# Kernel tuning notes

Hardware: AMD Instinct MI355X
Metric: run time of the kernel (lower is better)

## Reference

```python
import jax, jax.numpy as jnp
import numpy as np
import math

B, S, D, H, L, FF, T = 2, 1024, 1024, 16, 8, 4096, 512
HD = D // H
EPS = 1e-5


def _ln(x, g, b):
    m = jnp.mean(x, axis=-1, keepdims=True)
    v = jnp.var(x, axis=-1, keepdims=True)
    return (x - m) * jax.lax.rsqrt(v + EPS) * g + b


def _rope(x, cos, sin):
    # x: [B,S,H,HD]; interleaved even/odd rotary as in _apply_rotary_emb_sincos
    xe, xo = x[..., 0::2], x[..., 1::2]
    c = cos[None, :, None, :]
    s = sin[None, :, None, :]
    return jnp.stack([xe * c - xo * s, xe * s + xo * c], axis=-1).reshape(x.shape)


def setup_inputs():
    key = jax.random.key(0)
    ks = iter(jax.random.split(key, 40))
    n = lambda shape, sc=0.02: jax.random.normal(next(ks), shape, jnp.float32) * sc
    return {
        "inputs_embeds": jax.random.normal(next(ks), (B, S, D), jnp.float32),
        "attention_mask": jnp.ones((B, 1, 1, S), jnp.float32),
        "time_step": jax.random.uniform(next(ks), (B,), jnp.float32),
        "wpe": n((S, D)),
        "ln1_g": jnp.ones((L, D)), "ln1_b": jnp.zeros((L, D)),
        "attn_w": n((L, D, 3 * D)), "attn_b": jnp.zeros((L, 3 * D)),
        "projw": n((L, D, D)), "projb": jnp.zeros((L, D)),
        "ln2_g": jnp.ones((L, D)), "ln2_b": jnp.zeros((L, D)),
        "fcw": n((L, D, FF)), "fcb": jnp.zeros((L, FF)),
        "pw2": n((L, FF, D)), "pb2": jnp.zeros((L, D)),
        "sst": n((L, 6, D), 1.0 / D ** 0.5),
        "te_w1": n((T, D)), "te_b1": jnp.zeros((D,)),
        "te_w2": n((D, D)), "te_b2": jnp.zeros((D,)),
        "ada_w": n((D, 6 * D)), "ada_b": jnp.zeros((6 * D,)),
        "lnf_g": jnp.ones((D,)), "lnf_b": jnp.zeros((D,)),
        "fsst": n((2, D), 1.0 / D ** 0.5),
        "out_w": n((D, D)), "out_b": jnp.zeros((D,)),
    }


def reference(inputs_embeds, attention_mask, time_step, wpe, ln1_g, ln1_b,
              attn_w, attn_b, projw, projb, ln2_g, ln2_b, fcw, fcb, pw2, pb2,
              sst, te_w1, te_b1, te_w2, te_b2, ada_w, ada_b, lnf_g, lnf_b,
              fsst, out_w, out_b):
    hs = inputs_embeds + wpe[:S][None]  # position embedding
    # rotary tables: [S, HD//2]
    half = HD // 2
    freqs = 1.0 / (10000.0 ** (jnp.arange(half, dtype=jnp.float32) * 2.0 / HD))
    ang = jnp.arange(S, dtype=jnp.float32)[:, None] * freqs[None]
    cos, sin = jnp.cos(ang), jnp.sin(ang)
    mask = (1.0 - attention_mask) * jnp.finfo(jnp.float32).min  # [B,1,1,S]
    # timestep embedding (flow_t_size=T, scale=1000, max_period=10000)
    halfT = T // 2
    tf = jnp.exp(-math.log(10000.0) * jnp.arange(halfT, dtype=jnp.float32) / halfT)
    targs = time_step[:, None] * tf[None] * 1000.0
    tproj = jnp.concatenate([jnp.cos(targs), jnp.sin(targs)], axis=-1)  # [B,T]
    emb = jax.nn.silu(tproj @ te_w1 + te_b1) @ te_w2 + te_b2  # [B,D]
    adaln = (jax.nn.silu(emb) @ ada_w + ada_b).reshape(B, 6, D)

    layer_params = dict(ln1_g=ln1_g, ln1_b=ln1_b, aw=attn_w, ab=attn_b,
                        pw=projw, pb=projb, ln2_g=ln2_g, ln2_b=ln2_b,
                        fw=fcw, fb=fcb, qw=pw2, qb=pb2, sst=sst)

    def block(h, p):
        mod = p["sst"][None] + adaln  # [B,6,D]
        sh1, sc1, g1, sh2, sc2, g2 = [mod[:, i:i + 1] for i in range(6)]
        res = h
        x = _ln(h, p["ln1_g"], p["ln1_b"]) * (1.0 + sc1) + sh1
        qkv = x @ p["aw"] + p["ab"]
        q, k, v = [t.reshape(B, S, H, HD) for t in jnp.split(qkv, 3, axis=-1)]
        q, k = _rope(q, cos, sin), _rope(k, cos, sin)
        scores = jnp.einsum("bqhd,bkhd->bhqk", q, k) / math.sqrt(HD) + mask
        attn = jax.nn.softmax(scores, axis=-1)
        o = jnp.einsum("bhqk,bkhd->bqhd", attn, v).reshape(B, S, D)
        o = o @ p["pw"] + p["pb"]
        h = o * g1 + res
        res = h
        x = _ln(h, p["ln2_g"], p["ln2_b"]) * (1.0 + sc2) + sh2
        x = jax.nn.gelu(x @ p["fw"] + p["fb"], approximate=True) @ p["qw"] + p["qb"]
        return x * g2 + res, None

    hs, _ = jax.lax.scan(block, hs, layer_params)
    fmod = fsst[None] + emb[:, None]  # [B,2,D]
    shift, scale = fmod[:, 0:1], fmod[:, 1:2]
    hs = _ln(hs, lnf_g, lnf_b) * (1.0 + scale) + shift
    return hs @ out_w + out_b
```

## Files before the change

### kernel.cpp

```cpp
#include <hip/hip_runtime.h>
#include <stdint.h>

typedef unsigned short u16;
typedef __attribute__((ext_vector_type(8))) short bf8_t;
typedef __attribute__((ext_vector_type(4))) float f4_t;

#define DEV static __device__ __forceinline__
#define MFMA16(a, b, c) __builtin_amdgcn_mfma_f32_16x16x32_bf16((a), (b), (c), 0, 0, 0)
#define GLDS(gp, lp) __builtin_amdgcn_global_load_lds((const __attribute__((address_space(1))) void*)(gp), \
                                                      (__attribute__((address_space(3))) void*)(lp), 16, 0, 0)

DEV u16 f2bf(float f) {
  union { float f; uint32_t u; } x; x.f = f;
  uint32_t r = x.u + 0x7FFFu + ((x.u >> 16) & 1u);
  return (u16)(r >> 16);
}

DEV void transpose_body(const float* __restrict__ W, u16* __restrict__ WT, int K, int N,
                        int n0, int k0, u16 (*tl)[66]) {
  const int t = threadIdx.x;
  const int tx = t & 15, ty = t >> 4;
  #pragma unroll
  for (int i = 0; i < 64; i += 16) {
    const float4 v = *(const float4*)&W[(long)(k0 + ty + i) * N + n0 + tx * 4];
    tl[tx * 4 + 0][ty + i] = f2bf(v.x);
    tl[tx * 4 + 1][ty + i] = f2bf(v.y);
    tl[tx * 4 + 2][ty + i] = f2bf(v.z);
    tl[tx * 4 + 3][ty + i] = f2bf(v.w);
  }
  __syncthreads();
  const int c = t & 15, r = t >> 4;
  #pragma unroll
  for (int i = 0; i < 64; i += 16) {
    const u16* p = &tl[r + i][c * 4];
    uint2 w;
    w.x = (uint32_t)p[0] | ((uint32_t)p[1] << 16);
    w.y = (uint32_t)p[2] | ((uint32_t)p[3] << 16);
    *(uint2*)&WT[(long)(n0 + r + i) * K + k0 + c * 4] = w;
  }
}

__global__ __launch_bounds__(256) void transpose_k(const float* __restrict__ W, u16* __restrict__ WT,
                                                   int K, int N) {
  __shared__ u16 tl[64][66];
  transpose_body(W, WT, K, N, blockIdx.x * 64, blockIdx.y * 64, tl);
}

__global__ __launch_bounds__(256)
void transpose4_k(const float* __restrict__ w0, u16* __restrict__ o0,
                  const float* __restrict__ w1, u16* __restrict__ o1,
                  const float* __restrict__ w2, u16* __restrict__ o2,
                  const float* __restrict__ w3, u16* __restrict__ o3) {
  __shared__ u16 tl[64][66];
  int bid = blockIdx.x;
  const float* W; u16* O; int K, N, nbx;
  if (bid < 768)        {             W = w0; O = o0; K = 1024; N = 3072; nbx = 48; }
  else if (bid < 1024)  { bid -= 768; W = w1; O = o1; K = 1024; N = 1024; nbx = 16; }
  else if (bid < 2048)  { bid -= 1024; W = w2; O = o2; K = 1024; N = 4096; nbx = 64; }
  else                  { bid -= 2048; W = w3; O = o3; K = 4096; N = 1024; nbx = 16; }
  transpose_body(W, O, K, N, (bid % nbx) * 64, (bid / nbx) * 64, tl);
}

enum { EPI_F32 = 0, EPI_GATE = 1, EPI_GELU = 2, EPI_RAW = 3 };

template <int BM, int EPI, int KS>
__global__ __launch_bounds__(256)
void gemm_bt(const u16* __restrict__ A, const u16* __restrict__ BT, const float* __restrict__ bias,
             float* outF, u16* outB, const float* gate, const float* res, int M, int N, int K) {
  constexpr int MI = BM / 32;
  __shared__ u16 sA[BM * 32];
  __shared__ u16 sB[128 * 32];
  const int tid = threadIdx.x, lane = tid & 63, wid = tid >> 6;
  const long rowBase = (long)blockIdx.x * BM;
  const long colBase = (long)blockIdx.y * 128;
  const int kz = (KS > 1) ? blockIdx.z : 0;
  const int kbeg = kz * (K / KS), kend = kbeg + K / KS;
  const int wr = (wid >> 1) * (BM / 2), wc = (wid & 1) * 64;
  const int fr = lane & 15, kg = (lane >> 4) * 8;

  const f4_t zero = {0.0f, 0.0f, 0.0f, 0.0f};
  f4_t acc[MI][4];
  #pragma unroll
  for (int i = 0; i < MI; ++i)
    #pragma unroll
    for (int j = 0; j < 4; ++j) acc[i][j] = zero;

  const int sr = lane >> 2, scol = (lane & 3) * 8;
  const int c0 = wid * 2;
  const u16 *Ag0, *Ag1 = nullptr, *Bg0, *Bg1;
  u16 *lA0, *lA1 = nullptr, *lB0, *lB1;
  if constexpr (BM == 128) {
    Ag0 = A + (rowBase + c0 * 16 + sr) * (long)K + scol;
    Ag1 = A + (rowBase + c0 * 16 + 16 + sr) * (long)K + scol;
    lA0 = &sA[(c0 * 16) * 32];
    lA1 = &sA[(c0 * 16 + 16) * 32];
  } else {
    Ag0 = A + (rowBase + wid * 16 + sr) * (long)K + scol;
    lA0 = &sA[(wid * 16) * 32];
  }
  Bg0 = BT + (colBase + c0 * 16 + sr) * (long)K + scol;
  Bg1 = BT + (colBase + c0 * 16 + 16 + sr) * (long)K + scol;
  lB0 = &sB[(c0 * 16) * 32];
  lB1 = &sB[(c0 * 16 + 16) * 32];

  for (int k0 = kbeg; k0 < kend; k0 += 32) {
    GLDS(Ag0 + k0, lA0);
    if constexpr (BM == 128) GLDS(Ag1 + k0, lA1);
    GLDS(Bg0 + k0, lB0);
    GLDS(Bg1 + k0, lB1);
    __syncthreads();
    bf8_t af[MI], bfv[4];
    #pragma unroll
    for (int m = 0; m < MI; ++m) af[m] = *(const bf8_t*)&sA[(wr + m * 16 + fr) * 32 + kg];
    #pragma unroll
    for (int n = 0; n < 4; ++n) bfv[n] = *(const bf8_t*)&sB[(wc + n * 16 + fr) * 32 + kg];
    #pragma unroll
    for (int m = 0; m < MI; ++m)
      #pragma unroll
      for (int n = 0; n < 4; ++n) acc[m][n] = MFMA16(af[m], bfv[n], acc[m][n]);
    __syncthreads();
  }

  const int r0 = (lane >> 4) * 4;
  #pragma unroll
  for (int m = 0; m < MI; ++m) {
    #pragma unroll
    for (int n = 0; n < 4; ++n) {
      const long col = colBase + wc + n * 16 + fr;
      const float bv = (EPI == EPI_RAW) ? 0.0f : bias[col];
      #pragma unroll
      for (int j = 0; j < 4; ++j) {
        const long row = rowBase + wr + m * 16 + r0 + j;
        float v = acc[m][n][j] + bv;
        if (EPI == EPI_F32) {
          outF[row * N + col] = v;
        } else if (EPI == EPI_RAW) {
          outF[((long)kz * M + row) * N + col] = v;
        } else if (EPI == EPI_GATE) {
          const int b = (int)(row >> 10);
          const float g = gate[(long)b * 6144 + col];
          outF[row * N + col] = v * g + res[row * N + col];
        } else {
          const float t = 0.7978845608028654f * (v + 0.044715f * v * v * v);
          const float e = __expf(2.0f * t);
          const float th = 1.0f - 2.0f / (e + 1.0f);
          outB[row * N + col] = f2bf(0.5f * v * (1.0f + th));
        }
      }
    }
  }
}

__global__ __launch_bounds__(256)
void reduce_gate(const float* __restrict__ part, const float* __restrict__ bias,
                 const float* __restrict__ gate, float* __restrict__ hs) {
  const long i = (long)blockIdx.x * 256 + threadIdx.x;
  const long e0 = i * 4;
  const int col = (int)(e0 & 1023);
  const int row = (int)(e0 >> 10);
  const int b = row >> 10;
  const f4_t p = *(const f4_t*)&part[e0];
  const f4_t q = *(const f4_t*)&part[e0 + 2048ll * 1024];
  const f4_t bv = *(const f4_t*)&bias[col];
  const f4_t gv = *(const f4_t*)&gate[(long)b * 6144 + col];
  const f4_t r = *(const f4_t*)&hs[e0];
  f4_t o;
  #pragma unroll
  for (int j = 0; j < 4; ++j) o[j] = (p[j] + q[j] + bv[j]) * gv[j] + r[j];
  *(f4_t*)&hs[e0] = o;
}

__global__ __launch_bounds__(256)
void ln_mod(const float* __restrict__ h, const float* __restrict__ gamma, const float* __restrict__ beta,
            const float* shp, const float* scp, int bstride, u16* __restrict__ xb) {
  __shared__ float red[8];
  const int row = blockIdx.x;
  const int b = row >> 10;
  const int t = threadIdx.x;
  const float* hp = h + (long)row * 1024;
  float4 x = *(const float4*)&hp[t * 4];
  float s = x.x + x.y + x.z + x.w;
  #pragma unroll
  for (int o = 32; o > 0; o >>= 1) s += __shfl_down(s, o);
  const int lane = t & 63, wid = t >> 6;
  if (lane == 0) red[wid] = s;
  __syncthreads();
  const float mean = (red[0] + red[1] + red[2] + red[3]) * 0.0009765625f;
  const float d0 = x.x - mean, d1 = x.y - mean, d2 = x.z - mean, d3 = x.w - mean;
  float vs = d0 * d0 + d1 * d1 + d2 * d2 + d3 * d3;
  #pragma unroll
  for (int o = 32; o > 0; o >>= 1) vs += __shfl_down(vs, o);
  if (lane == 0) red[4 + wid] = vs;
  __syncthreads();
  const float var = (red[4] + red[5] + red[6] + red[7]) * 0.0009765625f;
  const float inv = rsqrtf(var + 1e-5f);
  const int d = t * 4;
  const float4 gg = *(const float4*)&gamma[d];
  const float4 bb = *(const float4*)&beta[d];
  const float4 sh = *(const float4*)&shp[(long)b * bstride + d];
  const float4 sc = *(const float4*)&scp[(long)b * bstride + d];
  union { u16 u[4]; uint2 v; } pk;
  pk.u[0] = f2bf((d0 * inv * gg.x + bb.x) * (1.0f + sc.x) + sh.x);
  pk.u[1] = f2bf((d1 * inv * gg.y + bb.y) * (1.0f + sc.y) + sh.y);
  pk.u[2] = f2bf((d2 * inv * gg.z + bb.z) * (1.0f + sc.z) + sh.z);
  pk.u[3] = f2bf((d3 * inv * gg.w + bb.w) * (1.0f + sc.w) + sh.w);
  *(uint2*)&xb[(long)row * 1024 + d] = pk.v;
}

__global__ __launch_bounds__(256)
void rope_split(const float* __restrict__ qkv, const float* __restrict__ ct, const float* __restrict__ st,
                u16* __restrict__ qb, u16* __restrict__ kb) {
  const int row = blockIdx.x;
  const int b = row >> 10, s = row & 1023;
  const float* rp = qkv + (long)row * 3072;
  const int t = threadIdx.x;
  #pragma unroll
  for (int which = 0; which < 2; ++which) {
    const float* xp = rp + which * 1024;
    u16* op = which ? kb : qb;
    #pragma unroll
    for (int j = 0; j < 2; ++j) {
      const int p = t + j * 256;
      const int h = p >> 5, i = p & 31;
      const float xe = xp[h * 64 + 2 * i], xo = xp[h * 64 + 2 * i + 1];
      const float c = ct[s * 32 + i], sn = st[s * 32 + i];
      const long base = (((long)(b * 16 + h)) * 1024 + s) * 64 + 2 * i;
      op[base] = f2bf(xe * c - xo * sn);
      op[base + 1] = f2bf(xe * sn + xo * c);
    }
  }
}

__global__ __launch_bounds__(256)
void v_transpose(const float* __restrict__ qkv, u16* __restrict__ vt) {
  __shared__ u16 tl[64][66];
  const int s0 = blockIdx.x * 64;
  const int h = blockIdx.y, b = blockIdx.z;
  const int t = threadIdx.x;
  const int tx = t & 15, ty = t >> 4;
  #pragma unroll
  for (int i = 0; i < 64; i += 16) {
    const float4 v = *(const float4*)&qkv[(long)(b * 1024 + s0 + ty + i) * 3072 + 2048 + h * 64 + tx * 4];
    tl[tx * 4 + 0][ty + i] = f2bf(v.x);
    tl[tx * 4 + 1][ty + i] = f2bf(v.y);
    tl[tx * 4 + 2][ty + i] = f2bf(v.z);
    tl[tx * 4 + 3][ty + i] = f2bf(v.w);
  }
  __syncthreads();
  const int c = t & 15, r = t >> 4;
  #pragma unroll
  for (int i = 0; i < 64; i += 16) {
    const u16* p = &tl[r + i][c * 4];
    uint2 w;
    w.x = (uint32_t)p[0] | ((uint32_t)p[1] << 16);
    w.y = (uint32_t)p[2] | ((uint32_t)p[3] << 16);
    *(uint2*)&vt[((long)(b * 16 + h) * 64 + r + i) * 1024 + s0 + c * 4] = w;
  }
}

DEV void attn_body(bf8_t (&kcur)[4][2], bf8_t (&knxt)[4][2], const bf8_t (&qf)[2],
                   f4_t (&oacc)[4], float& m, float& psum, int kc,
                   const u16* __restrict__ Kp, const u16* __restrict__ Vt,
                   const float* smadd, u16* myP, int fr, int g) {
  const f4_t zero = {0.0f, 0.0f, 0.0f, 0.0f};
  bf8_t vf[4][2];
  #pragma unroll
  for (int dt = 0; dt < 4; ++dt)
    #pragma unroll
    for (int ks = 0; ks < 2; ++ks)
      vf[dt][ks] = *(const bf8_t*)&Vt[(long)(dt * 16 + fr) * 1024 + kc + ks * 32 + g * 8];
  f4_t st[4];
  #pragma unroll
  for (int kt = 0; kt < 4; ++kt) {
    st[kt] = MFMA16(kcur[kt][0], qf[0], zero);
    st[kt] = MFMA16(kcur[kt][1], qf[1], st[kt]);
  }
  {
    const int kn = (kc + 64) & 1023;
    #pragma unroll
    for (int kt = 0; kt < 4; ++kt)
      #pragma unroll
      for (int dh = 0; dh < 2; ++dh)
        knxt[kt][dh] = *(const bf8_t*)&Kp[(long)(kn + kt * 16 + fr) * 64 + dh * 32 + g * 8];
  }
  float p[4][4];
  float cm = -3.402823466e38f;
  #pragma unroll
  for (int kt = 0; kt < 4; ++kt)
    #pragma unroll
    for (int j = 0; j < 4; ++j) {
      p[kt][j] = st[kt][j] * 0.125f + smadd[kc + kt * 16 + g * 4 + j];
      cm = fmaxf(cm, p[kt][j]);
    }
  cm = fmaxf(cm, __shfl_xor(cm, 16));
  cm = fmaxf(cm, __shfl_xor(cm, 32));
  const float nm = fmaxf(m, cm);
  const float sc = __expf(m - nm);
  m = nm;
  float ls = 0.0f;
  #pragma unroll
  for (int kt = 0; kt < 4; ++kt)
    #pragma unroll
    for (int j = 0; j < 4; ++j) {
      p[kt][j] = __expf(p[kt][j] - nm);
      ls += p[kt][j];
    }
  psum = psum * sc + ls;
  #pragma unroll
  for (int dt = 0; dt < 4; ++dt)
    #pragma unroll
    for (int j = 0; j < 4; ++j) oacc[dt][j] *= sc;
  #pragma unroll
  for (int kt = 0; kt < 4; ++kt) {
    const int kb = kt * 2 + (g >> 1);
    uint2 w;
    w.x = (uint32_t)f2bf(p[kt][0]) | ((uint32_t)f2bf(p[kt][1]) << 16);
    w.y = (uint32_t)f2bf(p[kt][2]) | ((uint32_t)f2bf(p[kt][3]) << 16);
    *(uint2*)&myP[(kb * 16 + fr) * 8 + (g & 1) * 4] = w;
  }
  bf8_t pa0 = *(const bf8_t*)&myP[(g * 16 + fr) * 8];
  bf8_t pa1 = *(const bf8_t*)&myP[((4 + g) * 16 + fr) * 8];
  #pragma unroll
  for (int dt = 0; dt < 4; ++dt) {
    oacc[dt] = MFMA16(vf[dt][0], pa0, oacc[dt]);
    oacc[dt] = MFMA16(vf[dt][1], pa1, oacc[dt]);
  }
}

__global__ __launch_bounds__(256)
void attn_k(const u16* __restrict__ qb, const u16* __restrict__ kb, const u16* __restrict__ vt,
            const float* __restrict__ amask, u16* __restrict__ ob) {
  __shared__ float smadd[1024];
  __shared__ u16 pl[4][1024];
  const int q0 = blockIdx.x * 64;
  const int h = blockIdx.y, b = blockIdx.z;
  const long bh = b * 16 + h;
  const int tid = threadIdx.x, lane = tid & 63, wid = tid >> 6;
  const int fr = lane & 15, g = lane >> 4;

  for (int i = tid; i < 1024; i += 256)
    smadd[i] = (1.0f - amask[b * 1024 + i]) * -3.402823466e38f;
  __syncthreads();

  const u16* Q = qb + (bh * 1024 + q0 + wid * 16) * 64;
  const u16* Kp = kb + bh * 1024 * 64;
  const u16* Vt = vt + bh * 64 * 1024;
  u16* myP = &pl[wid][0];

  bf8_t qf[2];
  qf[0] = *(const bf8_t*)&Q[fr * 64 + g * 8];
  qf[1] = *(const bf8_t*)&Q[fr * 64 + 32 + g * 8];

  const f4_t zero = {0.0f, 0.0f, 0.0f, 0.0f};
  f4_t oacc[4];
  #pragma unroll
  for (int dt = 0; dt < 4; ++dt) oacc[dt] = zero;
  float m = -1e30f, psum = 0.0f;

  bf8_t kfA[4][2], kfB[4][2];
  #pragma unroll
  for (int kt = 0; kt < 4; ++kt)
    #pragma unroll
    for (int dh = 0; dh < 2; ++dh)
      kfA[kt][dh] = *(const bf8_t*)&Kp[(long)(kt * 16 + fr) * 64 + dh * 32 + g * 8];

  for (int kc = 0; kc < 1024; kc += 128) {
    attn_body(kfA, kfB, qf, oacc, m, psum, kc, Kp, Vt, smadd, myP, fr, g);
    attn_body(kfB, kfA, qf, oacc, m, psum, kc + 64, Kp, Vt, smadd, myP, fr, g);
  }

  float ts = psum + __shfl_xor(psum, 16);
  ts += __shfl_xor(ts, 32);
  const float inv = 1.0f / ts;
  const long qrow = (long)b * 1024 + q0 + wid * 16 + fr;
  #pragma unroll
  for (int dt = 0; dt < 4; ++dt) {
    union { u16 u[4]; uint2 v; } pk;
    #pragma unroll
    for (int j = 0; j < 4; ++j) pk.u[j] = f2bf(oacc[dt][j] * inv);
    *(uint2*)&ob[qrow * 1024 + h * 64 + dt * 16 + g * 4] = pk.v;
  }
}

__global__ void rope_tables(float* ct, float* st) {
  const int i = blockIdx.x * 256 + threadIdx.x;
  const int s = i >> 5, k = i & 31;
  const float freq = __expf(-9.210340371976184f * (float)(2 * k) / 64.0f);
  const float a = (float)s * freq;
  ct[i] = cosf(a);
  st[i] = sinf(a);
}

__global__ void init_hs(const float* __restrict__ e, const float* __restrict__ wpe, float* __restrict__ hs) {
  const long i = (long)blockIdx.x * 256 + threadIdx.x;
  float4 a = ((const float4*)e)[i];
  const float4 w = ((const float4*)wpe)[i & 262143];
  a.x += w.x; a.y += w.y; a.z += w.z; a.w += w.w;
  ((float4*)hs)[i] = a;
}

__global__ void time_proj_k(const float* __restrict__ ts, float* __restrict__ tproj) {
  const int j = blockIdx.x * 256 + threadIdx.x;
  const int b = blockIdx.y;
  const float tf = __expf(-9.210340371976184f * (float)(j & 255) / 256.0f);
  const float a = ts[b] * tf * 1000.0f;
  tproj[b * 512 + j] = (j < 256) ? cosf(a) : sinf(a);
}

__global__ __launch_bounds__(256)
void time_mlp1(const float* __restrict__ tproj, const float* __restrict__ w1,
               const float* __restrict__ b1, float* __restrict__ h1) {
  __shared__ float red[8][32];
  const int dl = threadIdx.x & 31, sl = threadIdx.x >> 5;
  const int d = blockIdx.x * 32 + dl, b = blockIdx.y;
  float acc = 0.0f;
  for (int j = sl * 64; j < sl * 64 + 64; ++j) acc += tproj[b * 512 + j] * w1[(long)j * 1024 + d];
  red[sl][dl] = acc;
  __syncthreads();
  if (threadIdx.x < 32) {
    const int dd = blockIdx.x * 32 + threadIdx.x;
    float a = b1[dd];
    #pragma unroll
    for (int s = 0; s < 8; ++s) a += red[s][threadIdx.x];
    h1[b * 1024 + dd] = a / (1.0f + __expf(-a));
  }
}

__global__ __launch_bounds__(256)
void time_mlp2(const float* __restrict__ h1, const float* __restrict__ w2,
               const float* __restrict__ b2, float* __restrict__ emb) {
  __shared__ float red[8][32];
  const int dl = threadIdx.x & 31, sl = threadIdx.x >> 5;
  const int d = blockIdx.x * 32 + dl, b = blockIdx.y;
  float acc = 0.0f;
  for (int j = sl * 128; j < sl * 128 + 128; ++j) acc += h1[b * 1024 + j] * w2[(long)j * 1024 + d];
  red[sl][dl] = acc;
  __syncthreads();
  if (threadIdx.x < 32) {
    const int dd = blockIdx.x * 32 + threadIdx.x;
    float a = b2[dd];
    #pragma unroll
    for (int s = 0; s < 8; ++s) a += red[s][threadIdx.x];
    emb[b * 1024 + dd] = a;
  }
}

__global__ void silu_k(const float* __restrict__ in, float* __restrict__ out, int n) {
  const int i = blockIdx.x * 256 + threadIdx.x;
  if (i < n) { const float v = in[i]; out[i] = v / (1.0f + __expf(-v)); }
}

__global__ void adaln_part(const float* __restrict__ se, const float* __restrict__ aw,
                           float* __restrict__ part) {
  const int j = blockIdx.x * 256 + threadIdx.x;
  const int b = blockIdx.y, kz = blockIdx.z;
  float acc = 0.0f;
  for (int k = kz * 128; k < kz * 128 + 128; ++k) acc += se[b * 1024 + k] * aw[(long)k * 6144 + j];
  part[((long)kz * 2 + b) * 6144 + j] = acc;
}

__global__ void adaln_reduce(const float* __restrict__ part, const float* __restrict__ ab,
                             float* __restrict__ adaln) {
  const int j = blockIdx.x * 256 + threadIdx.x;
  const int b = blockIdx.y;
  float acc = ab[j];
  #pragma unroll
  for (int kz = 0; kz < 8; ++kz) acc += part[((long)kz * 2 + b) * 6144 + j];
  adaln[b * 6144 + j] = acc;
}

__global__ void build_mods(const float* __restrict__ sst, const float* __restrict__ adaln,
                           const float* __restrict__ fsst, const float* __restrict__ emb,
                           float* __restrict__ modAll, float* __restrict__ fmod) {
  const int i = blockIdx.x * 256 + threadIdx.x;
  if (i < 98304) {
    const int d = i & 1023;
    const int rest = i >> 10;
    const int slot = rest % 6;
    const int t2 = rest / 6;
    const int bb = t2 & 1, l = t2 >> 1;
    modAll[i] = sst[(long)(l * 6 + slot) * 1024 + d] + adaln[bb * 6144 + slot * 1024 + d];
  } else if (i < 98304 + 4096) {
    const int j = i - 98304;
    const int d = j & 1023;
    const int slot = (j >> 10) & 1;
    const int bb = j >> 11;
    fmod[j] = fsst[slot * 1024 + d] + emb[bb * 1024 + d];
  }
}

extern "C" void kernel_launch(void* const* d_in, const int* in_sizes, int n_in,
                              void* d_out, int out_size, void* d_ws, size_t ws_size,
                              hipStream_t stream) {
  const float* inp_emb = (const float*)d_in[0];
  const float* amask  = (const float*)d_in[1];
  const float* tstep  = (const float*)d_in[2];
  const float* wpe    = (const float*)d_in[3];
  const float* ln1_g  = (const float*)d_in[4];
  const float* ln1_b  = (const float*)d_in[5];
  const float* attn_w = (const float*)d_in[6];
  const float* attn_b = (const float*)d_in[7];
  const float* projw  = (const float*)d_in[8];
  const float* projb  = (const float*)d_in[9];
  const float* ln2_g  = (const float*)d_in[10];
  const float* ln2_b  = (const float*)d_in[11];
  const float* fcw    = (const float*)d_in[12];
  const float* fcb    = (const float*)d_in[13];
  const float* pw2    = (const float*)d_in[14];
  const float* pb2    = (const float*)d_in[15];
  const float* sst    = (const float*)d_in[16];
  const float* te_w1  = (const float*)d_in[17];
  const float* te_b1  = (const float*)d_in[18];
  const float* te_w2  = (const float*)d_in[19];
  const float* te_b2  = (const float*)d_in[20];
  const float* ada_w  = (const float*)d_in[21];
  const float* ada_b  = (const float*)d_in[22];
  const float* lnf_g  = (const float*)d_in[23];
  const float* lnf_b  = (const float*)d_in[24];
  const float* fsst   = (const float*)d_in[25];
  const float* out_w  = (const float*)d_in[26];
  const float* out_b  = (const float*)d_in[27];
  float* out = (float*)d_out;
  (void)in_sizes; (void)n_in; (void)out_size; (void)ws_size;

  char* wsb = (char*)d_ws;
  size_t off = 0;
  auto alloc = [&](size_t bytes) -> void* {
    void* p = wsb + off;
    off += (bytes + 255) & ~(size_t)255;
    return p;
  };
  u16* wtA = (u16*)alloc(3072ll * 1024 * 2);
  u16* wtP = (u16*)alloc(1024ll * 1024 * 2);
  u16* wtF = (u16*)alloc(4096ll * 1024 * 2);
  u16* wtQ = (u16*)alloc(1024ll * 4096 * 2);
  u16* wtO = (u16*)alloc(1024ll * 1024 * 2);
  float* hs   = (float*)alloc(2048ll * 1024 * 4);
  float* qkv  = (float*)alloc(2048ll * 3072 * 4);
  u16*   ffb  = (u16*)qkv;
  float* part = (float*)alloc(2ll * 2048 * 1024 * 4);
  u16* xb = (u16*)alloc(2048ll * 1024 * 2);
  u16* qb = (u16*)alloc(2048ll * 1024 * 2);
  u16* kb = (u16*)alloc(2048ll * 1024 * 2);
  u16* vt = (u16*)alloc(2048ll * 1024 * 2);
  u16* ob = (u16*)alloc(2048ll * 1024 * 2);
  float* ct    = (float*)alloc(32768 * 4);
  float* st    = (float*)alloc(32768 * 4);
  float* tproj = (float*)alloc(2 * 512 * 4);
  float* h1    = (float*)alloc(2 * 1024 * 4);
  float* emb   = (float*)alloc(2 * 1024 * 4);
  float* se    = (float*)alloc(2 * 1024 * 4);
  float* adaln = (float*)alloc(2 * 6144 * 4);
  float* modAll = (float*)alloc(8ll * 2 * 6 * 1024 * 4);
  float* fmod   = (float*)alloc(2 * 2 * 1024 * 4);

  rope_tables<<<128, 256, 0, stream>>>(ct, st);
  init_hs<<<2048, 256, 0, stream>>>(inp_emb, wpe, hs);
  time_proj_k<<<dim3(2, 2), 256, 0, stream>>>(tstep, tproj);
  time_mlp1<<<dim3(32, 2), 256, 0, stream>>>(tproj, te_w1, te_b1, h1);
  time_mlp2<<<dim3(32, 2), 256, 0, stream>>>(h1, te_w2, te_b2, emb);
  silu_k<<<8, 256, 0, stream>>>(emb, se, 2048);
  adaln_part<<<dim3(24, 2, 8), 256, 0, stream>>>(se, ada_w, part);
  adaln_reduce<<<dim3(24, 2), 256, 0, stream>>>(part, ada_b, adaln);
  build_mods<<<400, 256, 0, stream>>>(sst, adaln, fsst, emb, modAll, fmod);
  transpose_k<<<dim3(16, 16), 256, 0, stream>>>(out_w, wtO, 1024, 1024);

  for (int l = 0; l < 8; ++l) {
    const float* ml = modAll + (long)l * 12288;
    transpose4_k<<<3072, 256, 0, stream>>>(attn_w + (long)l * 1024 * 3072, wtA,
                                           projw + (long)l * 1024 * 1024, wtP,
                                           fcw + (long)l * 1024 * 4096, wtF,
                                           pw2 + (long)l * 4096 * 1024, wtQ);

    ln_mod<<<2048, 256, 0, stream>>>(hs, ln1_g + l * 1024, ln1_b + l * 1024,
                                     ml + 0 * 1024, ml + 1 * 1024, 6144, xb);
    gemm_bt<128, EPI_F32, 1><<<dim3(16, 24), 256, 0, stream>>>(xb, wtA, attn_b + l * 3072,
                                                               qkv, nullptr, nullptr, nullptr, 2048, 3072, 1024);
    rope_split<<<2048, 256, 0, stream>>>(qkv, ct, st, qb, kb);
    v_transpose<<<dim3(16, 16, 2), 256, 0, stream>>>(qkv, vt);
    attn_k<<<dim3(16, 16, 2), 256, 0, stream>>>(qb, kb, vt, amask, ob);
    gemm_bt<64, EPI_GATE, 1><<<dim3(32, 8), 256, 0, stream>>>(ob, wtP, projb + l * 1024,
                                                              hs, nullptr, ml + 2 * 1024, hs, 2048, 1024, 1024);
    ln_mod<<<2048, 256, 0, stream>>>(hs, ln2_g + l * 1024, ln2_b + l * 1024,
                                     ml + 3 * 1024, ml + 4 * 1024, 6144, xb);
    gemm_bt<128, EPI_GELU, 1><<<dim3(16, 32), 256, 0, stream>>>(xb, wtF, fcb + l * 4096,
                                                                nullptr, ffb, nullptr, nullptr, 2048, 4096, 1024);
    gemm_bt<128, EPI_RAW, 2><<<dim3(16, 8, 2), 256, 0, stream>>>(ffb, wtQ, nullptr,
                                                                 part, nullptr, nullptr, nullptr, 2048, 1024, 4096);
    reduce_gate<<<2048, 256, 0, stream>>>(part, pb2 + l * 1024, ml + 5 * 1024, hs);
  }

  ln_mod<<<2048, 256, 0, stream>>>(hs, lnf_g, lnf_b, fmod + 0, fmod + 1024, 2048, xb);
  gemm_bt<64, EPI_F32, 1><<<dim3(32, 8), 256, 0, stream>>>(xb, wtO, out_b,
                                                           out, nullptr, nullptr, nullptr, 2048, 1024, 1024);
}
```

Baseline: 1.951 ms.

## Double-buffer GEMM LDS, fuse reduce-gate with next LayerNorm, shrink attention blocks

Adds a two-buffer LDS pipeline to the bf16 GEMM so the next K-tile's global-to-LDS load is issued before the current tile's MFMAs. The FF2 split-K reduction is fused with the following LayerNorm (the next layer's ln1 or the final LN), which removes one read and write pass over the hidden state per layer. LayerNorm now runs one wave per row with xor-shuffle reductions instead of a block-wide reduction through shared memory. Attention switches to one-wave blocks of 16 query rows with vectorized mask loads, and the rope writes are packed into 32-bit stores. The GEMM loop keeps a single barrier per iteration, and since global_load_lds is asynchronous, whether the prefetch is properly waited on before it is read is a correctness risk.

After: 1.826 ms. 1.07x faster.

```diff
diff --git a/kernel.cpp b/kernel.cpp
--- a/kernel.cpp
+++ b/kernel.cpp
@@ -68,13 +68,13 @@
 void gemm_bt(const u16* __restrict__ A, const u16* __restrict__ BT, const float* __restrict__ bias,
              float* outF, u16* outB, const float* gate, const float* res, int M, int N, int K) {
   constexpr int MI = BM / 32;
-  __shared__ u16 sA[BM * 32];
-  __shared__ u16 sB[128 * 32];
+  __shared__ u16 sA[2][BM * 32];
+  __shared__ u16 sB[2][128 * 32];
   const int tid = threadIdx.x, lane = tid & 63, wid = tid >> 6;
   const long rowBase = (long)blockIdx.x * BM;
   const long colBase = (long)blockIdx.y * 128;
   const int kz = (KS > 1) ? blockIdx.z : 0;
-  const int kbeg = kz * (K / KS), kend = kbeg + K / KS;
+  const int kbeg = kz * (K / KS);
   const int wr = (wid >> 1) * (BM / 2), wc = (wid & 1) * 64;
   const int fr = lane & 15, kg = (lane >> 4) * 8;
 
@@ -88,37 +88,45 @@
   const int sr = lane >> 2, scol = (lane & 3) * 8;
   const int c0 = wid * 2;
   const u16 *Ag0, *Ag1 = nullptr, *Bg0, *Bg1;
-  u16 *lA0, *lA1 = nullptr, *lB0, *lB1;
+  int aoff0, aoff1 = 0, boff0, boff1;
   if constexpr (BM == 128) {
     Ag0 = A + (rowBase + c0 * 16 + sr) * (long)K + scol;
     Ag1 = A + (rowBase + c0 * 16 + 16 + sr) * (long)K + scol;
-    lA0 = &sA[(c0 * 16) * 32];
-    lA1 = &sA[(c0 * 16 + 16) * 32];
+    aoff0 = (c0 * 16) * 32;
+    aoff1 = (c0 * 16 + 16) * 32;
   } else {
     Ag0 = A + (rowBase + wid * 16 + sr) * (long)K + scol;
-    lA0 = &sA[(wid * 16) * 32];
+    aoff0 = (wid * 16) * 32;
   }
   Bg0 = BT + (colBase + c0 * 16 + sr) * (long)K + scol;
   Bg1 = BT + (colBase + c0 * 16 + 16 + sr) * (long)K + scol;
-  lB0 = &sB[(c0 * 16) * 32];
-  lB1 = &sB[(c0 * 16 + 16) * 32];
-
-  for (int k0 = kbeg; k0 < kend; k0 += 32) {
-    GLDS(Ag0 + k0, lA0);
-    if constexpr (BM == 128) GLDS(Ag1 + k0, lA1);
-    GLDS(Bg0 + k0, lB0);
-    GLDS(Bg1 + k0, lB1);
-    __syncthreads();
+  boff0 = (c0 * 16) * 32;
+  boff1 = (c0 * 16 + 16) * 32;
+
+  auto stage = [&](int buf, int k0) {
+    GLDS(Ag0 + k0, &sA[buf][aoff0]);
+    if constexpr (BM == 128) GLDS(Ag1 + k0, &sA[buf][aoff1]);
+    GLDS(Bg0 + k0, &sB[buf][boff0]);
+    GLDS(Bg1 + k0, &sB[buf][boff1]);
+  };
+
+  const int nk = (K / KS) / 32;
+  stage(0, kbeg);
+  __syncthreads();
+  int cur = 0;
+  for (int t = 0; t < nk; ++t) {
+    if (t + 1 < nk) stage(cur ^ 1, kbeg + (t + 1) * 32);
     bf8_t af[MI], bfv[4];
     #pragma unroll
-    for (int m = 0; m < MI; ++m) af[m] = *(const bf8_t*)&sA[(wr + m * 16 + fr) * 32 + kg];
-    #pragma unroll
-    for (int n = 0; n < 4; ++n) bfv[n] = *(const bf8_t*)&sB[(wc + n * 16 + fr) * 32 + kg];
+    for (int m = 0; m < MI; ++m) af[m] = *(const bf8_t*)&sA[cur][(wr + m * 16 + fr) * 32 + kg];
+    #pragma unroll
+    for (int n = 0; n < 4; ++n) bfv[n] = *(const bf8_t*)&sB[cur][(wc + n * 16 + fr) * 32 + kg];
     #pragma unroll
     for (int m = 0; m < MI; ++m)
       #pragma unroll
       for (int n = 0; n < 4; ++n) acc[m][n] = MFMA16(af[m], bfv[n], acc[m][n]);
     __syncthreads();
+    cur ^= 1;
   }
 
   const int r0 = (lane >> 4) * 4;
@@ -152,59 +160,95 @@
 }
 
 __global__ __launch_bounds__(256)
-void reduce_gate(const float* __restrict__ part, const float* __restrict__ bias,
-                 const float* __restrict__ gate, float* __restrict__ hs) {
-  const long i = (long)blockIdx.x * 256 + threadIdx.x;
-  const long e0 = i * 4;
-  const int col = (int)(e0 & 1023);
-  const int row = (int)(e0 >> 10);
-  const int b = row >> 10;
-  const f4_t p = *(const f4_t*)&part[e0];
-  const f4_t q = *(const f4_t*)&part[e0 + 2048ll * 1024];
-  const f4_t bv = *(const f4_t*)&bias[col];
-  const f4_t gv = *(const f4_t*)&gate[(long)b * 6144 + col];
-  const f4_t r = *(const f4_t*)&hs[e0];
-  f4_t o;
-  #pragma unroll
-  for (int j = 0; j < 4; ++j) o[j] = (p[j] + q[j] + bv[j]) * gv[j] + r[j];
-  *(f4_t*)&hs[e0] = o;
-}
-
-__global__ __launch_bounds__(256)
 void ln_mod(const float* __restrict__ h, const float* __restrict__ gamma, const float* __restrict__ beta,
             const float* shp, const float* scp, int bstride, u16* __restrict__ xb) {
-  __shared__ float red[8];
-  const int row = blockIdx.x;
+  const int row = blockIdx.x * 4 + (threadIdx.x >> 6);
+  const int lane = threadIdx.x & 63;
   const int b = row >> 10;
-  const int t = threadIdx.x;
-  const float* hp = h + (long)row * 1024;
-  float4 x = *(const float4*)&hp[t * 4];
-  float s = x.x + x.y + x.z + x.w;
-  #pragma unroll
-  for (int o = 32; o > 0; o >>= 1) s += __shfl_down(s, o);
-  const int lane = t & 63, wid = t >> 6;
-  if (lane == 0) red[wid] = s;
-  __syncthreads();
-  const float mean = (red[0] + red[1] + red[2] + red[3]) * 0.0009765625f;
-  const float d0 = x.x - mean, d1 = x.y - mean, d2 = x.z - mean, d3 = x.w - mean;
-  float vs = d0 * d0 + d1 * d1 + d2 * d2 + d3 * d3;
-  #pragma unroll
-  for (int o = 32; o > 0; o >>= 1) vs += __shfl_down(vs, o);
-  if (lane == 0) red[4 + wid] = vs;
-  __syncthreads();
-  const float var = (red[4] + red[5] + red[6] + red[7]) * 0.0009765625f;
-  const float inv = rsqrtf(var + 1e-5f);
-  const int d = t * 4;
-  const float4 gg = *(const float4*)&gamma[d];
-  const float4 bb = *(const float4*)&beta[d];
-  const float4 sh = *(const float4*)&shp[(long)b * bstride + d];
-  const float4 sc = *(const float4*)&scp[(long)b * bstride + d];
-  union { u16 u[4]; uint2 v; } pk;
-  pk.u[0] = f2bf((d0 * inv * gg.x + bb.x) * (1.0f + sc.x) + sh.x);
-  pk.u[1] = f2bf((d1 * inv * gg.y + bb.y) * (1.0f + sc.y) + sh.y);
-  pk.u[2] = f2bf((d2 * inv * gg.z + bb.z) * (1.0f + sc.z) + sh.z);
-  pk.u[3] = f2bf((d3 * inv * gg.w + bb.w) * (1.0f + sc.w) + sh.w);
-  *(uint2*)&xb[(long)row * 1024 + d] = pk.v;
+  const long base = (long)row * 1024;
+  f4_t x[4];
+  float s = 0.0f;
+  #pragma unroll
+  for (int j = 0; j < 4; ++j) {
+    x[j] = *(const f4_t*)&h[base + j * 256 + lane * 4];
+    s += x[j][0] + x[j][1] + x[j][2] + x[j][3];
+  }
+  #pragma unroll
+  for (int o = 32; o > 0; o >>= 1) s += __shfl_xor(s, o);
+  const float mean = s * 0.0009765625f;
+  float vs = 0.0f;
+  #pragma unroll
+  for (int j = 0; j < 4; ++j)
+    #pragma unroll
+    for (int e = 0; e < 4; ++e) { const float d = x[j][e] - mean; vs += d * d; }
+  #pragma unroll
+  for (int o = 32; o > 0; o >>= 1) vs += __shfl_xor(vs, o);
+  const float inv = rsqrtf(vs * 0.0009765625f + 1e-5f);
+  #pragma unroll
+  for (int j = 0; j < 4; ++j) {
+    const int col = j * 256 + lane * 4;
+    const f4_t gg = *(const f4_t*)&gamma[col];
+    const f4_t bb = *(const f4_t*)&beta[col];
+    const f4_t sh = *(const f4_t*)&shp[(long)b * bstride + col];
+    const f4_t sc = *(const f4_t*)&scp[(long)b * bstride + col];
+    union { u16 u[4]; uint2 v; } pk;
+    #pragma unroll
+    for (int e = 0; e < 4; ++e)
+      pk.u[e] = f2bf(((x[j][e] - mean) * inv * gg[e] + bb[e]) * (1.0f + sc[e]) + sh[e]);
+    *(uint2*)&xb[base + col] = pk.v;
+  }
+}
+
+__global__ __launch_bounds__(256)
+void reduce_gate_ln(const float* __restrict__ part, const float* __restrict__ bias,
+                    const float* __restrict__ gate, float* __restrict__ hs,
+                    const float* __restrict__ gamma, const float* __restrict__ beta,
+                    const float* shp, const float* scp, int bstride, u16* __restrict__ xb) {
+  const int row = blockIdx.x * 4 + (threadIdx.x >> 6);
+  const int lane = threadIdx.x & 63;
+  const int b = row >> 10;
+  const long base = (long)row * 1024;
+  f4_t v[4];
+  float s = 0.0f;
+  #pragma unroll
+  for (int j = 0; j < 4; ++j) {
+    const int col = j * 256 + lane * 4;
+    const f4_t p = *(const f4_t*)&part[base + col];
+    const f4_t q = *(const f4_t*)&part[2048ll * 1024 + base + col];
+    const f4_t bv = *(const f4_t*)&bias[col];
+    const f4_t gv = *(const f4_t*)&gate[(long)b * 6144 + col];
+    const f4_t r = *(const f4_t*)&hs[base + col];
+    f4_t o;
+    #pragma unroll
+    for (int e = 0; e < 4; ++e) o[e] = (p[e] + q[e] + bv[e]) * gv[e] + r[e];
+    *(f4_t*)&hs[base + col] = o;
+    v[j] = o;
+    s += o[0] + o[1] + o[2] + o[3];
+  }
+  #pragma unroll
+  for (int o = 32; o > 0; o >>= 1) s += __shfl_xor(s, o);
+  const float mean = s * 0.0009765625f;
+  float vs = 0.0f;
+  #pragma unroll
+  for (int j = 0; j < 4; ++j)
+    #pragma unroll
+    for (int e = 0; e < 4; ++e) { const float d = v[j][e] - mean; vs += d * d; }
+  #pragma unroll
+  for (int o = 32; o > 0; o >>= 1) vs += __shfl_xor(vs, o);
+  const float inv = rsqrtf(vs * 0.0009765625f + 1e-5f);
+  #pragma unroll
+  for (int j = 0; j < 4; ++j) {
+    const int col = j * 256 + lane * 4;
+    const f4_t gg = *(const f4_t*)&gamma[col];
+    const f4_t bb = *(const f4_t*)&beta[col];
+    const f4_t sh = *(const f4_t*)&shp[(long)b * bstride + col];
+    const f4_t sc = *(const f4_t*)&scp[(long)b * bstride + col];
+    union { u16 u[4]; uint2 v; } pk;
+    #pragma unroll
+    for (int e = 0; e < 4; ++e)
+      pk.u[e] = f2bf(((v[j][e] - mean) * inv * gg[e] + bb[e]) * (1.0f + sc[e]) + sh[e]);
+    *(uint2*)&xb[base + col] = pk.v;
+  }
 }
 
 __global__ __launch_bounds__(256)
@@ -222,11 +266,12 @@
     for (int j = 0; j < 2; ++j) {
       const int p = t + j * 256;
       const int h = p >> 5, i = p & 31;
-      const float xe = xp[h * 64 + 2 * i], xo = xp[h * 64 + 2 * i + 1];
+      const float2 xx = *(const float2*)&xp[h * 64 + 2 * i];
       const float c = ct[s * 32 + i], sn = st[s * 32 + i];
       const long base = (((long)(b * 16 + h)) * 1024 + s) * 64 + 2 * i;
-      op[base] = f2bf(xe * c - xo * sn);
-      op[base + 1] = f2bf(xe * sn + xo * c);
+      const uint32_t w = (uint32_t)f2bf(xx.x * c - xx.y * sn) |
+                         ((uint32_t)f2bf(xx.x * sn + xx.y * c) << 16);
+      *(uint32_t*)&op[base] = w;
     }
   }
 }
@@ -286,12 +331,14 @@
   float p[4][4];
   float cm = -3.402823466e38f;
   #pragma unroll
-  for (int kt = 0; kt < 4; ++kt)
+  for (int kt = 0; kt < 4; ++kt) {
+    const f4_t ma = *(const f4_t*)&smadd[kc + kt * 16 + g * 4];
     #pragma unroll
     for (int j = 0; j < 4; ++j) {
-      p[kt][j] = st[kt][j] * 0.125f + smadd[kc + kt * 16 + g * 4 + j];
+      p[kt][j] = st[kt][j] * 0.125f + ma[j];
       cm = fmaxf(cm, p[kt][j]);
     }
+  }
   cm = fmaxf(cm, __shfl_xor(cm, 16));
   cm = fmaxf(cm, __shfl_xor(cm, 32));
   const float nm = fmaxf(m, cm);
@@ -327,25 +374,30 @@
   }
 }
 
-__global__ __launch_bounds__(256)
+__global__ __launch_bounds__(64)
 void attn_k(const u16* __restrict__ qb, const u16* __restrict__ kb, const u16* __restrict__ vt,
             const float* __restrict__ amask, u16* __restrict__ ob) {
   __shared__ float smadd[1024];
-  __shared__ u16 pl[4][1024];
-  const int q0 = blockIdx.x * 64;
+  __shared__ u16 pl[1024];
+  const int q0 = blockIdx.x * 16;
   const int h = blockIdx.y, b = blockIdx.z;
   const long bh = b * 16 + h;
-  const int tid = threadIdx.x, lane = tid & 63, wid = tid >> 6;
+  const int lane = threadIdx.x;
   const int fr = lane & 15, g = lane >> 4;
 
-  for (int i = tid; i < 1024; i += 256)
-    smadd[i] = (1.0f - amask[b * 1024 + i]) * -3.402823466e38f;
-  __syncthreads();
-
-  const u16* Q = qb + (bh * 1024 + q0 + wid * 16) * 64;
+  #pragma unroll
+  for (int i = 0; i < 4; ++i) {
+    const int e = (lane + i * 64) * 4;
+    const f4_t am = *(const f4_t*)&amask[b * 1024 + e];
+    f4_t md;
+    #pragma unroll
+    for (int j = 0; j < 4; ++j) md[j] = (1.0f - am[j]) * -3.402823466e38f;
+    *(f4_t*)&smadd[e] = md;
+  }
+
+  const u16* Q = qb + (bh * 1024 + q0) * 64;
   const u16* Kp = kb + bh * 1024 * 64;
   const u16* Vt = vt + bh * 64 * 1024;
-  u16* myP = &pl[wid][0];
 
   bf8_t qf[2];
   qf[0] = *(const bf8_t*)&Q[fr * 64 + g * 8];
@@ -365,14 +417,14 @@
       kfA[kt][dh] = *(const bf8_t*)&Kp[(long)(kt * 16 + fr) * 64 + dh * 32 + g * 8];
 
   for (int kc = 0; kc < 1024; kc += 128) {
-    attn_body(kfA, kfB, qf, oacc, m, psum, kc, Kp, Vt, smadd, myP, fr, g);
-    attn_body(kfB, kfA, qf, oacc, m, psum, kc + 64, Kp, Vt, smadd, myP, fr, g);
+    attn_body(kfA, kfB, qf, oacc, m, psum, kc, Kp, Vt, smadd, pl, fr, g);
+    attn_body(kfB, kfA, qf, oacc, m, psum, kc + 64, Kp, Vt, smadd, pl, fr, g);
   }
 
   float ts = psum + __shfl_xor(psum, 16);
   ts += __shfl_xor(ts, 32);
   const float inv = 1.0f / ts;
-  const long qrow = (long)b * 1024 + q0 + wid * 16 + fr;
+  const long qrow = (long)b * 1024 + q0 + fr;
   #pragma unroll
   for (int dt = 0; dt < 4; ++dt) {
     union { u16 u[4]; uint2 v; } pk;
@@ -565,6 +617,8 @@
   build_mods<<<400, 256, 0, stream>>>(sst, adaln, fsst, emb, modAll, fmod);
   transpose_k<<<dim3(16, 16), 256, 0, stream>>>(out_w, wtO, 1024, 1024);
 
+  ln_mod<<<512, 256, 0, stream>>>(hs, ln1_g, ln1_b, modAll + 0 * 1024, modAll + 1 * 1024, 6144, xb);
+
   for (int l = 0; l < 8; ++l) {
     const float* ml = modAll + (long)l * 12288;
     transpose4_k<<<3072, 256, 0, stream>>>(attn_w + (long)l * 1024 * 3072, wtA,
@@ -572,25 +626,30 @@
                                            fcw + (long)l * 1024 * 4096, wtF,
                                            pw2 + (long)l * 4096 * 1024, wtQ);
 
-    ln_mod<<<2048, 256, 0, stream>>>(hs, ln1_g + l * 1024, ln1_b + l * 1024,
-                                     ml + 0 * 1024, ml + 1 * 1024, 6144, xb);
     gemm_bt<128, EPI_F32, 1><<<dim3(16, 24), 256, 0, stream>>>(xb, wtA, attn_b + l * 3072,
                                                                qkv, nullptr, nullptr, nullptr, 2048, 3072, 1024);
     rope_split<<<2048, 256, 0, stream>>>(qkv, ct, st, qb, kb);
     v_transpose<<<dim3(16, 16, 2), 256, 0, stream>>>(qkv, vt);
-    attn_k<<<dim3(16, 16, 2), 256, 0, stream>>>(qb, kb, vt, amask, ob);
+    attn_k<<<dim3(64, 16, 2), 64, 0, stream>>>(qb, kb, vt, amask, ob);
     gemm_bt<64, EPI_GATE, 1><<<dim3(32, 8), 256, 0, stream>>>(ob, wtP, projb + l * 1024,
                                                               hs, nullptr, ml + 2 * 1024, hs, 2048, 1024, 1024);
-    ln_mod<<<2048, 256, 0, stream>>>(hs, ln2_g + l * 1024, ln2_b + l * 1024,
-                                     ml + 3 * 1024, ml + 4 * 1024, 6144, xb);
+    ln_mod<<<512, 256, 0, stream>>>(hs, ln2_g + l * 1024, ln2_b + l * 1024,
+                                    ml + 3 * 1024, ml + 4 * 1024, 6144, xb);
     gemm_bt<128, EPI_GELU, 1><<<dim3(16, 32), 256, 0, stream>>>(xb, wtF, fcb + l * 4096,
                                                                 nullptr, ffb, nullptr, nullptr, 2048, 4096, 1024);
     gemm_bt<128, EPI_RAW, 2><<<dim3(16, 8, 2), 256, 0, stream>>>(ffb, wtQ, nullptr,
                                                                  part, nullptr, nullptr, nullptr, 2048, 1024, 4096);
-    reduce_gate<<<2048, 256, 0, stream>>>(part, pb2 + l * 1024, ml + 5 * 1024, hs);
-  }
-
-  ln_mod<<<2048, 256, 0, stream>>>(hs, lnf_g, lnf_b, fmod + 0, fmod + 1024, 2048, xb);
+    if (l < 7) {
+      const float* mln = modAll + (long)(l + 1) * 12288;
+      reduce_gate_ln<<<512, 256, 0, stream>>>(part, pb2 + l * 1024, ml + 5 * 1024, hs,
+                                              ln1_g + (l + 1) * 1024, ln1_b + (l + 1) * 1024,
+                                              mln + 0 * 1024, mln + 1 * 1024, 6144, xb);
+    } else {
+      reduce_gate_ln<<<512, 256, 0, stream>>>(part, pb2 + l * 1024, ml + 5 * 1024, hs,
+                                              lnf_g, lnf_b, fmod + 0, fmod + 1024, 2048, xb);
+    }
+  }
+
   gemm_bt<64, EPI_F32, 1><<<dim3(32, 8), 256, 0, stream>>>(xb, wtO, out_b,
                                                            out, nullptr, nullptr, nullptr, 2048, 1024, 1024);
 }
```
